# Kernel optimization log

Measured on AMD Instinct MI355X. Metric: run time of the kernel, lower is better.

Reference implementation:

```python
import jax, jax.numpy as jnp
import numpy as np

HE = 256  # encoder hidden
HD = 256  # decoder hidden


def _orthogonalize(enc):
    # Faithful to orthogonalize_encoder_inputs_new_new_new:
    # for each timestep i: buffer = x[i] - sum_{j<i} (x[i]*x[j])/(x[i]*x[i]) * x[i]
    # (all ops elementwise). The inner sum over j<i is an exclusive cumsum.
    x = jnp.transpose(enc, (1, 0, 2))                       # [T, B, H]
    s = jnp.cumsum(x, axis=0) - x                           # exclusive cumsum over j<i
    out = x - ((x * s) / (x * x)) * x                       # i=0: s=0 -> out=x
    return jnp.transpose(out, (0, 1, 2)), out               # keep [T,B,H] layout


def setup_inputs() -> dict:
    key = jax.random.key(0)
    k1, k2, k3, k4, k5 = jax.random.split(key, 5)
    B, TE, TD = 16, 128, 128
    # keras 'uniform' initializer = RandomUniform(-0.05, 0.05)
    return {
        "encoder_out_seq": jax.random.normal(k1, (B, TE, HE), dtype=jnp.float32),
        "decoder_out_seq": jax.random.normal(k2, (B, TD, HD), dtype=jnp.float32),
        "W_a": jax.random.uniform(k3, (HE, HE), jnp.float32, -0.05, 0.05),
        "U_a": jax.random.uniform(k4, (HD, HE), jnp.float32, -0.05, 0.05),
        "V_a": jax.random.uniform(k5, (HE, 1), jnp.float32, -0.05, 0.05),
    }


def reference(encoder_out_seq, decoder_out_seq, W_a, U_a, V_a):
    # Gram-Schmidt-style pass (math as in source; exactly vectorizable)
    x = jnp.transpose(encoder_out_seq, (1, 0, 2))           # [TE, B, H]
    s = jnp.cumsum(x, axis=0) - x                           # sum_{j<i} x[j]
    ortho = x - ((x * s) / (x * x)) * x                     # [TE, B, H]
    enc = jnp.transpose(ortho, (1, 0, 2))                   # [B, TE, H]

    # Bahdanau attention: the K.rnn steps carry no real state, so vectorize
    # over decoder time.
    was = jnp.einsum('beh,hk->bek', enc, W_a)               # [B, TE, H]
    uah = jnp.einsum('bdh,hk->bdk', decoder_out_seq, U_a)   # [B, TD, H]
    # tanh(S.Wa + h.Ua) . Va  -> energies [B, TD, TE]
    energy = jnp.einsum('bdeh,ho->bde',
                        jnp.tanh(was[:, None, :, :] + uah[:, :, None, :]),
                        V_a)
    e_outputs = jax.nn.softmax(energy, axis=-1)             # [B, TD, TE]
    c_outputs = jnp.einsum('bde,beh->bdh', e_outputs, enc)  # [B, TD, H]
    return c_outputs, e_outputs
```

## Files before the change

### kernel.cpp

```cpp
#include <hip/hip_runtime.h>
#include <cstddef>

#define Bq 16
#define TEq 128
#define TDq 128
#define Hq 256

#define kC2  2.8853900817779268f
#define kL2E 1.4426950408889634f

static __device__ __forceinline__ float fast_rcp(float x) {
#if __has_builtin(__builtin_amdgcn_rcpf)
    return __builtin_amdgcn_rcpf(x);
#else
    return 1.0f / x;
#endif
}

static __device__ __forceinline__ float fast_exp2(float x) {
#if __has_builtin(__builtin_amdgcn_exp2f)
    return __builtin_amdgcn_exp2f(x);
#else
    return exp2f(x);
#endif
}

__global__ __launch_bounds__(256) void k_ortho(const float* __restrict__ enc,
                                               float* __restrict__ out) {
    const int b = blockIdx.y;
    const int hg = blockIdx.x;
    const int tid = threadIdx.x;
    const int hl = tid & 31;
    const int ck = tid >> 5;
    const int h = (hg << 5) + hl;

    __shared__ float sums[8][33];

    const float* p = enc + ((size_t)b * TEq + ck * 16) * Hq + h;
    float xs[16];
#pragma unroll
    for (int i = 0; i < 16; ++i) xs[i] = p[(size_t)i * Hq];
    float tot = 0.0f;
#pragma unroll
    for (int i = 0; i < 16; ++i) tot += xs[i];
    sums[ck][hl] = tot;
    __syncthreads();

    float s = 0.0f;
    for (int c = 0; c < ck; ++c) s += sums[c][hl];

    float* q = out + ((size_t)b * TEq + ck * 16) * Hq + h;
#pragma unroll
    for (int i = 0; i < 16; ++i) {
        const float x = xs[i];
        const float r = (x * s) / (x * x);
        q[(size_t)i * Hq] = x - r * x;
        s += x;
    }
}

__global__ __launch_bounds__(256) void k_gemm2(const float* __restrict__ A0,
                                               const float* __restrict__ A1,
                                               const float* __restrict__ W0,
                                               const float* __restrict__ W1,
                                               float* __restrict__ Cw,
                                               float* __restrict__ Cu) {
    const int z = blockIdx.z;
    const float* __restrict__ A = z ? A1 : A0;
    const float* __restrict__ W = z ? W1 : W0;
    float* __restrict__ C = z ? Cu : Cw;
    const float scale = z ? 1.0f : kC2;

    const int bm = blockIdx.y * 64;
    const int bn = blockIdx.x * 64;

    __shared__ float sA[32][68];

    const int tid = threadIdx.x;
    const int tx = tid & 15;
    const int ty = tid >> 4;
    const int sr = tid & 63;
    const int sc = (tid >> 6) << 2;

    const float* __restrict__ Bp = W + bn + (tx << 2);
    const float* __restrict__ Ap = A + (size_t)(bm + sr) * Hq;

    float acc[4][4] = {};
    float4 bcur[8], bnxt[8];

#pragma unroll
    for (int i = 0; i < 8; ++i)
        bcur[i] = *(const float4*)(Bp + (size_t)i * Hq);

    for (int kt = 0; kt < 8; ++kt) {
        const int k0 = kt * 32;
        const float4 a0 = *(const float4*)(Ap + k0 + sc);
        const float4 a1 = *(const float4*)(Ap + k0 + sc + 16);
        __syncthreads();
        sA[sc + 0][sr] = a0.x;  sA[sc + 1][sr] = a0.y;
        sA[sc + 2][sr] = a0.z;  sA[sc + 3][sr] = a0.w;
        sA[sc + 16][sr] = a1.x; sA[sc + 17][sr] = a1.y;
        sA[sc + 18][sr] = a1.z; sA[sc + 19][sr] = a1.w;
        __syncthreads();

#pragma unroll
        for (int kg = 0; kg < 4; ++kg) {
            const int nk = k0 + kg * 8 + 8;
            if (nk < Hq) {
#pragma unroll
                for (int i = 0; i < 8; ++i)
                    bnxt[i] = *(const float4*)(Bp + (size_t)(nk + i) * Hq);
            }
#pragma unroll
            for (int i = 0; i < 8; ++i) {
                const float4 a4 = *(const float4*)&sA[kg * 8 + i][ty << 2];
                const float af[4] = {a4.x, a4.y, a4.z, a4.w};
                const float bf[4] = {bcur[i].x, bcur[i].y, bcur[i].z, bcur[i].w};
#pragma unroll
                for (int r = 0; r < 4; ++r)
#pragma unroll
                    for (int c = 0; c < 4; ++c)
                        acc[r][c] = fmaf(af[r], bf[c], acc[r][c]);
            }
            if (nk < Hq) {
#pragma unroll
                for (int i = 0; i < 8; ++i) bcur[i] = bnxt[i];
            }
        }
    }

#pragma unroll
    for (int r = 0; r < 4; ++r) {
        float4 o;
        o.x = acc[r][0] * scale;
        o.y = acc[r][1] * scale;
        o.z = acc[r][2] * scale;
        o.w = acc[r][3] * scale;
        *(float4*)(C + (size_t)(bm + (ty << 2) + r) * Hq + bn + (tx << 2)) = o;
    }
}

__global__ __launch_bounds__(256) void k_attn(const float* __restrict__ was,
                                              const float* __restrict__ uah,
                                              const float* __restrict__ enc_o,
                                              const float* __restrict__ Va,
                                              float* __restrict__ c_out,
                                              float* __restrict__ e_out) {
    const int b = blockIdx.y;
    const int d0 = blockIdx.x << 1;

    __shared__ float uahs[2][Hq];
    __shared__ float Vs[Hq];
    __shared__ float wts[2][TEq];

    const int tid = threadIdx.x;
    const int w = tid >> 6;
    const int lane = tid & 63;
    const int dl = w >> 1;
    const int half = w & 1;

    Vs[tid] = Va[tid];
#pragma unroll
    for (int j = 0; j < 2; ++j)
        uahs[j][tid] = uah[((size_t)b * TDq + d0 + j) * Hq + tid] * kC2;
    __syncthreads();

    const int g = lane >> 4;
    const int ll = lane & 15;

    float vs = Vs[lane] + Vs[lane + 64] + Vs[lane + 128] + Vs[lane + 192];
#pragma unroll
    for (int m = 1; m <= 32; m <<= 1) vs += __shfl_xor(vs, m);

    float4 ur[4], vr[4];
#pragma unroll
    for (int c = 0; c < 4; ++c) {
        ur[c] = *(const float4*)&uahs[dl][c * 64 + (ll << 2)];
        vr[c] = *(const float4*)&Vs[c * 64 + (ll << 2)];
    }

    const float* wasb = was + (size_t)b * TEq * Hq;

    for (int ei = 0; ei < 16; ++ei) {
        const int e = (half << 6) + (g << 4) + ei;
        const float* wp = wasb + (size_t)e * Hq + (ll << 2);
        float acc = 0.0f;
#pragma unroll
        for (int c = 0; c < 4; ++c) {
            const float4 wv = *(const float4*)(wp + c * 64);
            const float wf[4] = {wv.x, wv.y, wv.z, wv.w};
            const float uf[4] = {ur[c].x, ur[c].y, ur[c].z, ur[c].w};
            const float vf[4] = {vr[c].x, vr[c].y, vr[c].z, vr[c].w};
#pragma unroll
            for (int i = 0; i < 4; ++i) {
                const float s = wf[i] + uf[i];
                const float t = fast_exp2(s);
                const float r = fast_rcp(t + 1.0f);
                acc = fmaf(vf[i], r, acc);
            }
        }
        acc += __shfl_xor(acc, 1);
        acc += __shfl_xor(acc, 2);
        acc += __shfl_xor(acc, 4);
        acc += __shfl_xor(acc, 8);
        if (ll == 0) wts[dl][e] = vs - 2.0f * acc;
    }
    __syncthreads();

    if (w < 2) {
        const float v0 = wts[w][lane];
        const float v1 = wts[w][lane + 64];
        float mx = fmaxf(v0, v1);
#pragma unroll
        for (int m = 1; m <= 32; m <<= 1) mx = fmaxf(mx, __shfl_xor(mx, m));
        const float e0 = fast_exp2((v0 - mx) * kL2E);
        const float e1 = fast_exp2((v1 - mx) * kL2E);
        float sm = e0 + e1;
#pragma unroll
        for (int m = 1; m <= 32; m <<= 1) sm += __shfl_xor(sm, m);
        const float inv = fast_rcp(sm);
        const float w0 = e0 * inv;
        const float w1 = e1 * inv;
        wts[w][lane] = w0;
        wts[w][lane + 64] = w1;
        const size_t eb = ((size_t)b * TDq + d0 + w) * TEq;
        e_out[eb + lane] = w0;
        e_out[eb + lane + 64] = w1;
    }
    __syncthreads();

    float a0 = 0.0f, a1 = 0.0f;
    const float* ep = enc_o + (size_t)b * TEq * Hq + tid;
#pragma unroll 4
    for (int e4 = 0; e4 < TEq; e4 += 4) {
        const float4 w0v = *(const float4*)&wts[0][e4];
        const float4 w1v = *(const float4*)&wts[1][e4];
        const float x0 = ep[(size_t)(e4 + 0) * Hq];
        const float x1 = ep[(size_t)(e4 + 1) * Hq];
        const float x2 = ep[(size_t)(e4 + 2) * Hq];
        const float x3 = ep[(size_t)(e4 + 3) * Hq];
        a0 = fmaf(w0v.x, x0, a0); a1 = fmaf(w1v.x, x0, a1);
        a0 = fmaf(w0v.y, x1, a0); a1 = fmaf(w1v.y, x1, a1);
        a0 = fmaf(w0v.z, x2, a0); a1 = fmaf(w1v.z, x2, a1);
        a0 = fmaf(w0v.w, x3, a0); a1 = fmaf(w1v.w, x3, a1);
    }
    const size_t cb = ((size_t)b * TDq + d0) * Hq + tid;
    c_out[cb] = a0;
    c_out[cb + Hq] = a1;
}

extern "C" void kernel_launch(void* const* d_in, const int* in_sizes, int n_in,
                              void* d_out, int out_size, void* d_ws, size_t ws_size,
                              hipStream_t stream) {
    const float* enc = (const float*)d_in[0];
    const float* dec = (const float*)d_in[1];
    const float* Wa  = (const float*)d_in[2];
    const float* Ua  = (const float*)d_in[3];
    const float* Va  = (const float*)d_in[4];

    float* c_out = (float*)d_out;
    float* e_out = c_out + (size_t)Bq * TDq * Hq;

    float* enc_o = (float*)d_ws;
    float* wasb  = enc_o + (size_t)Bq * TEq * Hq;
    float* uahb  = wasb + (size_t)Bq * TEq * Hq;

    k_ortho<<<dim3(Hq / 32, Bq), dim3(256), 0, stream>>>(enc, enc_o);
    k_gemm2<<<dim3(Hq / 64, (Bq * TEq) / 64, 2), dim3(256), 0, stream>>>(
        enc_o, dec, Wa, Ua, wasb, uahb);
    k_attn<<<dim3(TDq / 2, Bq), dim3(256), 0, stream>>>(
        wasb, uahb, enc_o, Va, c_out, e_out);
}
```

Measured before the change: 108.4 us.

## Register-tile gemm without LDS and widen attention blocks to eight decoder rows

The projection GEMM drops its shared-memory staging of A. Each thread now loads its own A rows and B columns straight into registers, double-buffered in 8-deep k chunks. The attention kernel moves from 2 to 8 decoder positions per 512-thread block, and each warp evaluates two decoder rows per loaded W_a·enc vector. This reuses each was read across more decoder rows and reduces how often enc_o is re-read for the context sum. The costs are higher register pressure, fewer blocks (256 vs 1024), and uncoalesced per-thread A loads in the GEMM.

```diff
diff --git a/kernel.cpp b/kernel.cpp
--- a/kernel.cpp
+++ b/kernel.cpp
@@ -74,60 +74,56 @@
     const int bm = blockIdx.y * 64;
     const int bn = blockIdx.x * 64;
 
-    __shared__ float sA[32][68];
-
     const int tid = threadIdx.x;
     const int tx = tid & 15;
     const int ty = tid >> 4;
-    const int sr = tid & 63;
-    const int sc = (tid >> 6) << 2;
-
+
+    const float* __restrict__ Ap = A + (size_t)(bm + (ty << 2)) * Hq;
     const float* __restrict__ Bp = W + bn + (tx << 2);
-    const float* __restrict__ Ap = A + (size_t)(bm + sr) * Hq;
 
     float acc[4][4] = {};
-    float4 bcur[8], bnxt[8];
-
-#pragma unroll
-    for (int i = 0; i < 8; ++i)
-        bcur[i] = *(const float4*)(Bp + (size_t)i * Hq);
-
-    for (int kt = 0; kt < 8; ++kt) {
-        const int k0 = kt * 32;
-        const float4 a0 = *(const float4*)(Ap + k0 + sc);
-        const float4 a1 = *(const float4*)(Ap + k0 + sc + 16);
-        __syncthreads();
-        sA[sc + 0][sr] = a0.x;  sA[sc + 1][sr] = a0.y;
-        sA[sc + 2][sr] = a0.z;  sA[sc + 3][sr] = a0.w;
-        sA[sc + 16][sr] = a1.x; sA[sc + 17][sr] = a1.y;
-        sA[sc + 18][sr] = a1.z; sA[sc + 19][sr] = a1.w;
-        __syncthreads();
-
-#pragma unroll
-        for (int kg = 0; kg < 4; ++kg) {
-            const int nk = k0 + kg * 8 + 8;
-            if (nk < Hq) {
-#pragma unroll
-                for (int i = 0; i < 8; ++i)
-                    bnxt[i] = *(const float4*)(Bp + (size_t)(nk + i) * Hq);
-            }
-#pragma unroll
-            for (int i = 0; i < 8; ++i) {
-                const float4 a4 = *(const float4*)&sA[kg * 8 + i][ty << 2];
-                const float af[4] = {a4.x, a4.y, a4.z, a4.w};
-                const float bf[4] = {bcur[i].x, bcur[i].y, bcur[i].z, bcur[i].w};
-#pragma unroll
-                for (int r = 0; r < 4; ++r)
-#pragma unroll
-                    for (int c = 0; c < 4; ++c)
-                        acc[r][c] = fmaf(af[r], bf[c], acc[r][c]);
-            }
-            if (nk < Hq) {
-#pragma unroll
-                for (int i = 0; i < 8; ++i) bcur[i] = bnxt[i];
-            }
-        }
-    }
+    float4 aA[8], bA[8], aB[8], bB[8];
+
+#define LOADC(ab, bb, k)                                                     \
+    {                                                                        \
+        _Pragma("unroll")                                                    \
+        for (int r = 0; r < 4; ++r) {                                        \
+            ab[r * 2 + 0] = *(const float4*)(Ap + (size_t)r * Hq + (k));     \
+            ab[r * 2 + 1] = *(const float4*)(Ap + (size_t)r * Hq + (k) + 4); \
+        }                                                                    \
+        _Pragma("unroll")                                                    \
+        for (int i = 0; i < 8; ++i)                                          \
+            bb[i] = *(const float4*)(Bp + (size_t)((k) + i) * Hq);           \
+    }
+
+#define COMPC(ab, bb)                                                        \
+    {                                                                        \
+        _Pragma("unroll")                                                    \
+        for (int q = 0; q < 2; ++q)                                          \
+            _Pragma("unroll")                                                \
+            for (int kk = 0; kk < 4; ++kk) {                                 \
+                const float4 bv = bb[q * 4 + kk];                            \
+                const float bf[4] = {bv.x, bv.y, bv.z, bv.w};                \
+                _Pragma("unroll")                                            \
+                for (int r = 0; r < 4; ++r) {                                \
+                    const float av = (&ab[r * 2 + q].x)[kk];                 \
+                    _Pragma("unroll")                                        \
+                    for (int c = 0; c < 4; ++c)                              \
+                        acc[r][c] = fmaf(av, bf[c], acc[r][c]);              \
+                }                                                            \
+            }                                                                \
+    }
+
+    LOADC(aA, bA, 0);
+#pragma unroll 1
+    for (int k = 0; k < Hq; k += 16) {
+        if (k + 8 < Hq) LOADC(aB, bB, k + 8);
+        COMPC(aA, bA);
+        if (k + 16 < Hq) LOADC(aA, bA, k + 16);
+        COMPC(aB, bB);
+    }
+#undef LOADC
+#undef COMPC
 
 #pragma unroll
     for (int r = 0; r < 4; ++r) {
@@ -140,29 +136,31 @@
     }
 }
 
-__global__ __launch_bounds__(256) void k_attn(const float* __restrict__ was,
+__global__ __launch_bounds__(512) void k_attn(const float* __restrict__ was,
                                               const float* __restrict__ uah,
                                               const float* __restrict__ enc_o,
                                               const float* __restrict__ Va,
                                               float* __restrict__ c_out,
                                               float* __restrict__ e_out) {
     const int b = blockIdx.y;
-    const int d0 = blockIdx.x << 1;
-
-    __shared__ float uahs[2][Hq];
+    const int d0 = blockIdx.x << 3;
+
+    __shared__ float uahs[8][Hq];
     __shared__ float Vs[Hq];
-    __shared__ float wts[2][TEq];
+    __shared__ float wts[8][TEq];
 
     const int tid = threadIdx.x;
     const int w = tid >> 6;
     const int lane = tid & 63;
-    const int dl = w >> 1;
-    const int half = w & 1;
-
-    Vs[tid] = Va[tid];
-#pragma unroll
-    for (int j = 0; j < 2; ++j)
-        uahs[j][tid] = uah[((size_t)b * TDq + d0 + j) * Hq + tid] * kC2;
+    const int p = w & 3;
+    const int half = w >> 2;
+
+    if (tid < Hq) Vs[tid] = Va[tid];
+    {
+        const int hcol = tid & 255;
+        for (int j = tid >> 8; j < 8; j += 2)
+            uahs[j][hcol] = uah[((size_t)b * TDq + d0 + j) * Hq + hcol] * kC2;
+    }
     __syncthreads();
 
     const int g = lane >> 4;
@@ -172,10 +170,11 @@
 #pragma unroll
     for (int m = 1; m <= 32; m <<= 1) vs += __shfl_xor(vs, m);
 
-    float4 ur[4], vr[4];
+    float4 u0[4], u1[4], vr[4];
 #pragma unroll
     for (int c = 0; c < 4; ++c) {
-        ur[c] = *(const float4*)&uahs[dl][c * 64 + (ll << 2)];
+        u0[c] = *(const float4*)&uahs[2 * p][c * 64 + (ll << 2)];
+        u1[c] = *(const float4*)&uahs[2 * p + 1][c * 64 + (ll << 2)];
         vr[c] = *(const float4*)&Vs[c * 64 + (ll << 2)];
     }
 
@@ -184,30 +183,36 @@
     for (int ei = 0; ei < 16; ++ei) {
         const int e = (half << 6) + (g << 4) + ei;
         const float* wp = wasb + (size_t)e * Hq + (ll << 2);
-        float acc = 0.0f;
+        float acc0 = 0.0f, acc1 = 0.0f;
 #pragma unroll
         for (int c = 0; c < 4; ++c) {
             const float4 wv = *(const float4*)(wp + c * 64);
             const float wf[4] = {wv.x, wv.y, wv.z, wv.w};
-            const float uf[4] = {ur[c].x, ur[c].y, ur[c].z, ur[c].w};
+            const float u0f[4] = {u0[c].x, u0[c].y, u0[c].z, u0[c].w};
+            const float u1f[4] = {u1[c].x, u1[c].y, u1[c].z, u1[c].w};
             const float vf[4] = {vr[c].x, vr[c].y, vr[c].z, vr[c].w};
 #pragma unroll
             for (int i = 0; i < 4; ++i) {
-                const float s = wf[i] + uf[i];
-                const float t = fast_exp2(s);
-                const float r = fast_rcp(t + 1.0f);
-                acc = fmaf(vf[i], r, acc);
+                const float s0 = wf[i] + u0f[i];
+                const float t0 = fast_exp2(s0);
+                acc0 = fmaf(vf[i], fast_rcp(t0 + 1.0f), acc0);
+                const float s1 = wf[i] + u1f[i];
+                const float t1 = fast_exp2(s1);
+                acc1 = fmaf(vf[i], fast_rcp(t1 + 1.0f), acc1);
             }
         }
-        acc += __shfl_xor(acc, 1);
-        acc += __shfl_xor(acc, 2);
-        acc += __shfl_xor(acc, 4);
-        acc += __shfl_xor(acc, 8);
-        if (ll == 0) wts[dl][e] = vs - 2.0f * acc;
-    }
-    __syncthreads();
-
-    if (w < 2) {
+        acc0 += __shfl_xor(acc0, 1); acc1 += __shfl_xor(acc1, 1);
+        acc0 += __shfl_xor(acc0, 2); acc1 += __shfl_xor(acc1, 2);
+        acc0 += __shfl_xor(acc0, 4); acc1 += __shfl_xor(acc1, 4);
+        acc0 += __shfl_xor(acc0, 8); acc1 += __shfl_xor(acc1, 8);
+        if (ll == 0) {
+            wts[2 * p][e]     = vs - 2.0f * acc0;
+            wts[2 * p + 1][e] = vs - 2.0f * acc1;
+        }
+    }
+    __syncthreads();
+
+    {
         const float v0 = wts[w][lane];
         const float v1 = wts[w][lane + 64];
         float mx = fmaxf(v0, v1);
@@ -229,24 +234,34 @@
     }
     __syncthreads();
 
-    float a0 = 0.0f, a1 = 0.0f;
-    const float* ep = enc_o + (size_t)b * TEq * Hq + tid;
+    const int h = tid & 255;
+    const int db = (tid >> 8) << 2;
+    float a0 = 0.0f, a1 = 0.0f, a2 = 0.0f, a3 = 0.0f;
+    const float* ep = enc_o + (size_t)b * TEq * Hq + h;
 #pragma unroll 4
     for (int e4 = 0; e4 < TEq; e4 += 4) {
-        const float4 w0v = *(const float4*)&wts[0][e4];
-        const float4 w1v = *(const float4*)&wts[1][e4];
+        const float4 w0v = *(const float4*)&wts[db + 0][e4];
+        const float4 w1v = *(const float4*)&wts[db + 1][e4];
+        const float4 w2v = *(const float4*)&wts[db + 2][e4];
+        const float4 w3v = *(const float4*)&wts[db + 3][e4];
         const float x0 = ep[(size_t)(e4 + 0) * Hq];
         const float x1 = ep[(size_t)(e4 + 1) * Hq];
         const float x2 = ep[(size_t)(e4 + 2) * Hq];
         const float x3 = ep[(size_t)(e4 + 3) * Hq];
         a0 = fmaf(w0v.x, x0, a0); a1 = fmaf(w1v.x, x0, a1);
+        a2 = fmaf(w2v.x, x0, a2); a3 = fmaf(w3v.x, x0, a3);
         a0 = fmaf(w0v.y, x1, a0); a1 = fmaf(w1v.y, x1, a1);
+        a2 = fmaf(w2v.y, x1, a2); a3 = fmaf(w3v.y, x1, a3);
         a0 = fmaf(w0v.z, x2, a0); a1 = fmaf(w1v.z, x2, a1);
+        a2 = fmaf(w2v.z, x2, a2); a3 = fmaf(w3v.z, x2, a3);
         a0 = fmaf(w0v.w, x3, a0); a1 = fmaf(w1v.w, x3, a1);
-    }
-    const size_t cb = ((size_t)b * TDq + d0) * Hq + tid;
-    c_out[cb] = a0;
-    c_out[cb + Hq] = a1;
+        a2 = fmaf(w2v.w, x3, a2); a3 = fmaf(w3v.w, x3, a3);
+    }
+    const size_t cb = ((size_t)b * TDq + d0 + db) * Hq + h;
+    c_out[cb]           = a0;
+    c_out[cb + Hq]      = a1;
+    c_out[cb + 2 * Hq]  = a2;
+    c_out[cb + 3 * Hq]  = a3;
 }
 
 extern "C" void kernel_launch(void* const* d_in, const int* in_sizes, int n_in,
@@ -268,6 +283,6 @@
     k_ortho<<<dim3(Hq / 32, Bq), dim3(256), 0, stream>>>(enc, enc_o);
     k_gemm2<<<dim3(Hq / 64, (Bq * TEq) / 64, 2), dim3(256), 0, stream>>>(
         enc_o, dec, Wa, Ua, wasb, uahb);
-    k_attn<<<dim3(TDq / 2, Bq), dim3(256), 0, stream>>>(
+    k_attn<<<dim3(TDq / 8, Bq), dim3(512), 0, stream>>>(
         wasb, uahb, enc_o, Va, c_out, e_out);
 }
```

Measured after the change: 111.3 us. 2.8% more time.
